# Kernel optimization log

Measured on AMD Instinct MI355X. Metric: run time of the kernel, lower is better.

## Reference

```python
import jax, jax.numpy as jnp
import numpy as np

B, S, H, NH = 2, 2048, 1024, 16
HD = H // NH  # 64


def setup_inputs() -> dict:
    key = jax.random.key(0)
    ks = jax.random.split(key, 9)
    w = lambda k: jax.random.normal(k, (H, H), dtype=jnp.float32) * 0.02  # torch Linear weight [out,in]
    b = lambda k: jax.random.normal(k, (H,), dtype=jnp.float32) * 0.02
    return {
        "hidden_states": jax.random.normal(ks[0], (B, S, H), dtype=jnp.float32),
        "Wq": w(ks[1]), "bq": b(ks[2]),
        "Wk": w(ks[3]), "bk": b(ks[4]),
        "Wv": w(ks[5]), "bv": b(ks[6]),
        "Wo": w(ks[7]), "bo": b(ks[8]),
    }


def reference(hidden_states, Wq, bq, Wk, bk, Wv, bv, Wo, bo):
    b, s, h = hidden_states.shape
    nh, hd = NH, h // NH

    def proj(W, bias):
        y = hidden_states @ W.T + bias  # torch Linear: x W^T + b
        return y.reshape(b, s, nh, hd).transpose(0, 2, 1, 3)  # [b, h, s, d]

    q = proj(Wq, bq)
    k = proj(Wk, bk)
    v = proj(Wv, bv)

    scale = jnp.sqrt(jnp.asarray(hd, dtype=q.dtype))
    scores = jnp.einsum("bhqd,bhkd->bhqk", q, k) / scale  # [b, h, s, s]
    pos = jnp.arange(s)
    causal = pos[:, None] < pos[None, :]  # True where masked (key after query)
    scores = jnp.where(causal[None, None], -jnp.inf, scores)
    attn = jax.nn.softmax(scores, axis=-1)
    out = jnp.einsum("bhqk,bhkd->bhqd", attn, v)
    out = out.transpose(0, 2, 1, 3).reshape(b, s, h)
    return out @ Wo.T + bo
```

## Files before the change

kernel.cpp:

```cpp
#include <hip/hip_runtime.h>
#include <stdint.h>

typedef __bf16 bf16;
typedef __attribute__((ext_vector_type(2))) __bf16 bf16x2;
typedef __attribute__((ext_vector_type(4))) __bf16 bf16x4;
typedef __attribute__((ext_vector_type(8))) __bf16 bf16x8;
typedef __attribute__((ext_vector_type(4))) float f32x4;

#define B_  2
#define S_  2048
#define H_  1024
#define NH_ 16
#define HD_ 64
#define ST  72
#define STV 136

__global__ __launch_bounds__(256) void cvt_f32_bf16(
    const float* __restrict__ s0, bf16* __restrict__ d0, int n0,
    const float* __restrict__ s1, bf16* __restrict__ d1,
    const float* __restrict__ s2, bf16* __restrict__ d2,
    const float* __restrict__ s3, bf16* __restrict__ d3,
    const float* __restrict__ s4, bf16* __restrict__ d4, int nw)
{
  const float* s; bf16* d; int n;
  switch (blockIdx.y) {
    case 0:  s = s0; d = d0; n = n0; break;
    case 1:  s = s1; d = d1; n = nw; break;
    case 2:  s = s2; d = d2; n = nw; break;
    case 3:  s = s3; d = d3; n = nw; break;
    default: s = s4; d = d4; n = nw; break;
  }
  const int i = (blockIdx.x * 256 + threadIdx.x) * 8;
  if (i >= n) return;
  float4 v0 = *(const float4*)(s + i);
  float4 v1 = *(const float4*)(s + i + 4);
  bf16x8 o;
  o[0] = (bf16)v0.x; o[1] = (bf16)v0.y; o[2] = (bf16)v0.z; o[3] = (bf16)v0.w;
  o[4] = (bf16)v1.x; o[5] = (bf16)v1.y; o[6] = (bf16)v1.z; o[7] = (bf16)v1.w;
  *(bf16x8*)(d + i) = o;
}

template <typename TY>
__global__ __launch_bounds__(256) void gemm_bt_bias(
    const bf16* __restrict__ X,
    const bf16* __restrict__ W0, const bf16* __restrict__ W1, const bf16* __restrict__ W2,
    const float* __restrict__ b0, const float* __restrict__ b1, const float* __restrict__ b2,
    TY* __restrict__ Y0, TY* __restrict__ Y1, TY* __restrict__ Y2,
    int M, int N, int K)
{
  const bf16* W; const float* bias; TY* Y;
  if (blockIdx.z == 0)      { W = W0; bias = b0; Y = Y0; }
  else if (blockIdx.z == 1) { W = W1; bias = b1; Y = Y1; }
  else                      { W = W2; bias = b2; Y = Y2; }

  __shared__ __align__(16) bf16 As[128 * 32];
  __shared__ __align__(16) bf16 Bs[128 * 32];

  const int tid  = threadIdx.x;
  const int lane = tid & 63;
  const int wave = tid >> 6;
  const int m0 = blockIdx.y * 128;
  const int n0 = blockIdx.x * 128;
  const int wm = (wave >> 1) * 64;
  const int wn = (wave & 1) * 64;

  f32x4 acc[4][4] = {};
  bf16x8 pa[2], pb[2];

#pragma unroll
  for (int it = 0; it < 2; ++it) {
    const int c = it * 256 + tid, row = c >> 2, col = (c & 3) * 8;
    pa[it] = *(const bf16x8*)(X + (size_t)(m0 + row) * K + col);
    pb[it] = *(const bf16x8*)(W + (size_t)(n0 + row) * K + col);
  }

  for (int k0 = 0; k0 < K; k0 += 32) {
    __syncthreads();
#pragma unroll
    for (int it = 0; it < 2; ++it) {
      const int c = it * 256 + tid, row = c >> 2, col = (c & 3) * 8;
      *(bf16x8*)&As[row * 32 + col] = pa[it];
      *(bf16x8*)&Bs[row * 32 + col] = pb[it];
    }
    __syncthreads();

    if (k0 + 32 < K) {
#pragma unroll
      for (int it = 0; it < 2; ++it) {
        const int c = it * 256 + tid, row = c >> 2, col = (c & 3) * 8;
        pa[it] = *(const bf16x8*)(X + (size_t)(m0 + row) * K + k0 + 32 + col);
        pb[it] = *(const bf16x8*)(W + (size_t)(n0 + row) * K + k0 + 32 + col);
      }
    }

    bf16x8 a[4], b[4];
#pragma unroll
    for (int i = 0; i < 4; ++i)
      a[i] = *(const bf16x8*)&As[(wm + i * 16 + (lane & 15)) * 32 + (lane >> 4) * 8];
#pragma unroll
    for (int i = 0; i < 4; ++i)
      b[i] = *(const bf16x8*)&Bs[(wn + i * 16 + (lane & 15)) * 32 + (lane >> 4) * 8];
#pragma unroll
    for (int mi = 0; mi < 4; ++mi)
#pragma unroll
      for (int ni = 0; ni < 4; ++ni)
        acc[mi][ni] = __builtin_amdgcn_mfma_f32_16x16x32_bf16(a[mi], b[ni], acc[mi][ni], 0, 0, 0);
  }

#pragma unroll
  for (int mi = 0; mi < 4; ++mi) {
    const int row = m0 + wm + mi * 16 + (lane >> 4) * 4;
#pragma unroll
    for (int ni = 0; ni < 4; ++ni) {
      const int col = n0 + wn + ni * 16 + (lane & 15);
      const float bv = bias[col];
#pragma unroll
      for (int r = 0; r < 4; ++r)
        Y[(size_t)(row + r) * N + col] = (TY)(acc[mi][ni][r] + bv);
    }
  }
}

__global__ __launch_bounds__(256) void attn_causal(
    const bf16* __restrict__ Q, const bf16* __restrict__ K,
    const bf16* __restrict__ V, bf16* __restrict__ O)
{
  const int pair = blockIdx.x;
  const int bh   = blockIdx.y;
  const int b    = bh >> 4;
  const int h    = bh & 15;

  const int tid  = threadIdx.x;
  const int lane = tid & 63;
  const int wave = tid >> 6;
  const int quad = lane >> 4;
  const int l15  = lane & 15;
  const size_t headoff = (size_t)b * S_ * H_ + (size_t)h * HD_;

  __shared__ __align__(16) bf16 Qs[64 * ST];
  __shared__ __align__(16) bf16 Ks[128 * ST];
  __shared__ __align__(16) bf16 Vt[64 * STV];
  __shared__ __align__(16) bf16 Ps[4][16 * STV];

  for (int phase = 0; phase < 2; ++phase) {
    const int qt = phase ? (31 - pair) : pair;
    const int q0 = qt * 64;
    __syncthreads();

#pragma unroll
    for (int it = 0; it < 2; ++it) {
      const int c = it * 256 + tid, row = c >> 3, col = (c & 7) * 8;
      *(bf16x8*)&Qs[row * ST + col] =
          *(const bf16x8*)(Q + headoff + (size_t)(q0 + row) * H_ + col);
    }

    const int qrow = q0 + wave * 16 + l15;
    float mr = -1e30f, lr = 0.0f;
    f32x4 oacc[4] = {};

    const int niter = (qt >> 1) + 1;
    for (int it = 0; it < niter; ++it) {
      const int k0 = it * 128;
      __syncthreads();

#pragma unroll
      for (int j = 0; j < 4; ++j) {
        const int c = j * 256 + tid, row = c >> 3, col = (c & 7) * 8;
        *(bf16x8*)&Ks[row * ST + col] =
            *(const bf16x8*)(K + headoff + (size_t)(k0 + row) * H_ + col);
      }
      {
        const int vr = (tid & 63) * 2;
        const int vc = (tid >> 6) * 16;
        bf16x8 a0 = *(const bf16x8*)(V + headoff + (size_t)(k0 + vr) * H_ + vc);
        bf16x8 a1 = *(const bf16x8*)(V + headoff + (size_t)(k0 + vr) * H_ + vc + 8);
        bf16x8 c0 = *(const bf16x8*)(V + headoff + (size_t)(k0 + vr + 1) * H_ + vc);
        bf16x8 c1 = *(const bf16x8*)(V + headoff + (size_t)(k0 + vr + 1) * H_ + vc + 8);
#pragma unroll
        for (int e = 0; e < 8; ++e) {
          bf16x2 p0; p0[0] = a0[e]; p0[1] = c0[e];
          *(bf16x2*)&Vt[(vc + e) * STV + vr] = p0;
          bf16x2 p1; p1[0] = a1[e]; p1[1] = c1[e];
          *(bf16x2*)&Vt[(vc + 8 + e) * STV + vr] = p1;
        }
      }
      __syncthreads();

      f32x4 sacc[8] = {};
#pragma unroll
      for (int ks = 0; ks < 2; ++ks) {
        bf16x8 bq = *(const bf16x8*)&Qs[(wave * 16 + l15) * ST + ks * 32 + quad * 8];
#pragma unroll
        for (int mb = 0; mb < 8; ++mb) {
          bf16x8 ak = *(const bf16x8*)&Ks[(mb * 16 + l15) * ST + ks * 32 + quad * 8];
          sacc[mb] = __builtin_amdgcn_mfma_f32_16x16x32_bf16(ak, bq, sacc[mb], 0, 0, 0);
        }
      }

      float sv[8][4];
#pragma unroll
      for (int mb = 0; mb < 8; ++mb) {
        const int kb = k0 + mb * 16 + quad * 4;
#pragma unroll
        for (int r = 0; r < 4; ++r) {
          const float s = sacc[mb][r] * 0.125f;
          sv[mb][r] = (kb + r > qrow) ? -1e30f : s;
        }
      }

      float mx = -1e30f;
#pragma unroll
      for (int mb = 0; mb < 8; ++mb)
        mx = fmaxf(mx, fmaxf(fmaxf(sv[mb][0], sv[mb][1]), fmaxf(sv[mb][2], sv[mb][3])));
      mx = fmaxf(mx, __shfl_xor(mx, 16, 64));
      mx = fmaxf(mx, __shfl_xor(mx, 32, 64));
      const float mnew  = fmaxf(mr, mx);
      const float alpha = __expf(mr - mnew);
      mr = mnew;

      float sum = 0.0f;
#pragma unroll
      for (int mb = 0; mb < 8; ++mb) {
        bf16x4 pw;
#pragma unroll
        for (int r = 0; r < 4; ++r) {
          const float p = __expf(sv[mb][r] - mnew);
          sum += p;
          pw[r] = (bf16)p;
        }
        *(bf16x4*)&Ps[wave][l15 * STV + mb * 16 + quad * 4] = pw;
      }
      sum += __shfl_xor(sum, 16, 64);
      sum += __shfl_xor(sum, 32, 64);
      lr = lr * alpha + sum;
#pragma unroll
      for (int mb = 0; mb < 4; ++mb)
#pragma unroll
        for (int r = 0; r < 4; ++r) oacc[mb][r] *= alpha;

#pragma unroll
      for (int ks = 0; ks < 4; ++ks) {
        bf16x8 bp = *(const bf16x8*)&Ps[wave][l15 * STV + ks * 32 + quad * 8];
#pragma unroll
        for (int mb = 0; mb < 4; ++mb) {
          bf16x8 av = *(const bf16x8*)&Vt[(mb * 16 + l15) * STV + ks * 32 + quad * 8];
          oacc[mb] = __builtin_amdgcn_mfma_f32_16x16x32_bf16(av, bp, oacc[mb], 0, 0, 0);
        }
      }
    }

    const float inv = 1.0f / lr;
#pragma unroll
    for (int mb = 0; mb < 4; ++mb) {
      bf16x4 o;
#pragma unroll
      for (int r = 0; r < 4; ++r) o[r] = (bf16)(oacc[mb][r] * inv);
      *(bf16x4*)(O + headoff + (size_t)qrow * H_ + mb * 16 + quad * 4) = o;
    }
  }
}

extern "C" void kernel_launch(void* const* d_in, const int* in_sizes, int n_in,
                              void* d_out, int out_size, void* d_ws, size_t ws_size,
                              hipStream_t stream) {
  const float* hs = (const float*)d_in[0];
  const float* Wq = (const float*)d_in[1]; const float* bq = (const float*)d_in[2];
  const float* Wk = (const float*)d_in[3]; const float* bk = (const float*)d_in[4];
  const float* Wv = (const float*)d_in[5]; const float* bv = (const float*)d_in[6];
  const float* Wo = (const float*)d_in[7]; const float* bo = (const float*)d_in[8];
  float* out = (float*)d_out;

  const size_t elems = (size_t)B_ * S_ * H_;
  const size_t wel   = (size_t)H_ * H_;
  bf16* hsb = (bf16*)d_ws;
  bf16* AO  = hsb;
  bf16* Wqb = hsb + elems;
  bf16* Wkb = Wqb + wel;
  bf16* Wvb = Wkb + wel;
  bf16* Wob = Wvb + wel;
  bf16* Qw  = Wob + wel;
  bf16* Kw  = Qw + elems;
  bf16* Vw  = Kw + elems;

  cvt_f32_bf16<<<dim3(2048, 5), dim3(256), 0, stream>>>(
      hs, hsb, (int)elems, Wq, Wqb, Wk, Wkb, Wv, Wvb, Wo, Wob, (int)wel);

  const int M = B_ * S_;
  gemm_bt_bias<bf16><<<dim3(H_ / 128, M / 128, 3), dim3(256), 0, stream>>>(
      hsb, Wqb, Wkb, Wvb, bq, bk, bv, Qw, Kw, Vw, M, H_, H_);

  attn_causal<<<dim3(16, B_ * NH_), dim3(256), 0, stream>>>(Qw, Kw, Vw, AO);

  gemm_bt_bias<float><<<dim3(H_ / 128, M / 128, 1), dim3(256), 0, stream>>>(
      AO, Wob, Wob, Wob, bo, bo, bo, out, out, out, M, H_, H_);
}
```

Measured before the change: 205.6 us.

## Use direct global-to-LDS loads in GEMM and exp2 softmax with masking only on diagonal

The projection GEMM now loads tiles with global_load_lds straight into shared memory instead of staging them through registers. This drops the register prefetch of the next tile, so load latency is no longer overlapped with compute. The attention kernel folds log2(e) into the score scale and uses the hardware exp2 builtin. It also applies the causal mask only on the last (diagonal) key tile, removing compare/select work on the other tiles.

```diff
diff --git a/kernel.cpp b/kernel.cpp
--- a/kernel.cpp
+++ b/kernel.cpp
@@ -14,6 +14,12 @@
 #define HD_ 64
 #define ST  72
 #define STV 136
+
+__device__ __forceinline__ void glds16(const bf16* g, bf16* l) {
+  __builtin_amdgcn_global_load_lds(
+      (const __attribute__((address_space(1))) uint32_t*)g,
+      (__attribute__((address_space(3))) uint32_t*)l, 16, 0, 0);
+}
 
 __global__ __launch_bounds__(256) void cvt_f32_bf16(
     const float* __restrict__ s0, bf16* __restrict__ d0, int n0,
@@ -65,33 +71,19 @@
   const int wn = (wave & 1) * 64;
 
   f32x4 acc[4][4] = {};
-  bf16x8 pa[2], pb[2];
-
-#pragma unroll
-  for (int it = 0; it < 2; ++it) {
-    const int c = it * 256 + tid, row = c >> 2, col = (c & 3) * 8;
-    pa[it] = *(const bf16x8*)(X + (size_t)(m0 + row) * K + col);
-    pb[it] = *(const bf16x8*)(W + (size_t)(n0 + row) * K + col);
-  }
 
   for (int k0 = 0; k0 < K; k0 += 32) {
     __syncthreads();
 #pragma unroll
     for (int it = 0; it < 2; ++it) {
-      const int c = it * 256 + tid, row = c >> 2, col = (c & 3) * 8;
-      *(bf16x8*)&As[row * 32 + col] = pa[it];
-      *(bf16x8*)&Bs[row * 32 + col] = pb[it];
+      const int c   = it * 256 + tid;
+      const int row = c >> 2;
+      const int col = (c & 3) * 8;
+      const int cb  = (it * 256 + wave * 64) * 8;
+      glds16(X + (size_t)(m0 + row) * K + k0 + col, As + cb);
+      glds16(W + (size_t)(n0 + row) * K + k0 + col, Bs + cb);
     }
     __syncthreads();
-
-    if (k0 + 32 < K) {
-#pragma unroll
-      for (int it = 0; it < 2; ++it) {
-        const int c = it * 256 + tid, row = c >> 2, col = (c & 3) * 8;
-        pa[it] = *(const bf16x8*)(X + (size_t)(m0 + row) * K + k0 + 32 + col);
-        pb[it] = *(const bf16x8*)(W + (size_t)(n0 + row) * K + k0 + 32 + col);
-      }
-    }
 
     bf16x8 a[4], b[4];
 #pragma unroll
@@ -136,6 +128,7 @@
   const int quad = lane >> 4;
   const int l15  = lane & 15;
   const size_t headoff = (size_t)b * S_ * H_ + (size_t)h * HD_;
+  const float SCL = 0.125f * 1.44269504f;
 
   __shared__ __align__(16) bf16 Qs[64 * ST];
   __shared__ __align__(16) bf16 Ks[128 * ST];
@@ -198,14 +191,22 @@
       }
 
       float sv[8][4];
-#pragma unroll
-      for (int mb = 0; mb < 8; ++mb) {
-        const int kb = k0 + mb * 16 + quad * 4;
-#pragma unroll
-        for (int r = 0; r < 4; ++r) {
-          const float s = sacc[mb][r] * 0.125f;
-          sv[mb][r] = (kb + r > qrow) ? -1e30f : s;
-        }
+      if (it == niter - 1) {
+#pragma unroll
+        for (int mb = 0; mb < 8; ++mb) {
+          const int kb = k0 + mb * 16 + quad * 4;
+#pragma unroll
+          for (int r = 0; r < 4; ++r) {
+            const float s = sacc[mb][r] * SCL;
+            sv[mb][r] = (kb + r > qrow) ? -1e30f : s;
+          }
+        }
+      } else {
+#pragma unroll
+        for (int mb = 0; mb < 8; ++mb)
+#pragma unroll
+          for (int r = 0; r < 4; ++r)
+            sv[mb][r] = sacc[mb][r] * SCL;
       }
 
       float mx = -1e30f;
@@ -215,7 +216,7 @@
       mx = fmaxf(mx, __shfl_xor(mx, 16, 64));
       mx = fmaxf(mx, __shfl_xor(mx, 32, 64));
       const float mnew  = fmaxf(mr, mx);
-      const float alpha = __expf(mr - mnew);
+      const float alpha = __builtin_amdgcn_exp2f(mr - mnew);
       mr = mnew;
 
       float sum = 0.0f;
@@ -224,7 +225,7 @@
         bf16x4 pw;
 #pragma unroll
         for (int r = 0; r < 4; ++r) {
-          const float p = __expf(sv[mb][r] - mnew);
+          const float p = __builtin_amdgcn_exp2f(sv[mb][r] - mnew);
           sum += p;
           pw[r] = (bf16)p;
         }
```

Result: slower. 211.0 us (+2.7%).
